# Optimization experiments

Hardware: AMD Instinct MI355X
Metric: run time of the kernel (lower is better)

The kernel has to match this reference:

```python
import jax, jax.numpy as jnp
import numpy as np

NEG_INF = -9e15
ALPHA = 2.0  # LeakyReLU negative slope from init (alpha=2)


def setup_inputs() -> dict:
    key = jax.random.key(0)
    k1, k2, k3, k4 = jax.random.split(key, 4)
    B, N, Fin, Fout = 8, 2048, 256, 128
    x = jax.random.normal(k1, (B, N, Fin), dtype=jnp.float32)
    adj = jax.random.randint(k2, (B, N, N), 0, 2, dtype=jnp.int32)
    # xavier_uniform with gain=1.414
    def xavier(k, shape, gain=1.414):
        fan_in, fan_out = shape[0], shape[1]
        bound = gain * np.sqrt(6.0 / (fan_in + fan_out))
        return jax.random.uniform(k, shape, jnp.float32, -bound, bound)
    W = xavier(k3, (Fin, Fout))
    a = xavier(k4, (2 * Fout, 1))
    return {"x": x, "adj": adj, "W": W, "a": a}


def reference(x, adj, W, a):
    # Wh: [B, N, Fout]
    Wh = jnp.matmul(x, W)
    Fout = W.shape[1]
    a1 = a[:Fout, 0]   # [Fout]
    a2 = a[Fout:, 0]   # [Fout]
    f1 = jnp.einsum('bnf,f->bn', Wh, a1)  # [B, N]
    f2 = jnp.einsum('bnf,f->bn', Wh, a2)  # [B, N]
    e = f1[:, :, None] + f2[:, None, :]   # [B, N, N]
    e = jnp.where(e >= 0, e, ALPHA * e)   # leaky relu, slope 2
    e = jnp.where(adj > 0, e, NEG_INF)
    attention = jax.nn.softmax(e, axis=2)
    # dropout: eval mode (no-op)
    h_prime = jnp.matmul(attention, Wh)   # [B, N, Fout]
    # concat=True -> elu
    return jnp.where(h_prime > 0, h_prime, jnp.expm1(h_prime))
```

## Files before the change

kernel.cpp:

```cpp
#include <hip/hip_runtime.h>
#include <hip/hip_bf16.h>
#include <math.h>

constexpr int B_   = 8;
constexpr int N_   = 2048;
constexpr int FIN  = 256;
constexpr int FOUT = 128;

constexpr int CH  = 512;
constexpr int NCH = N_ / CH;
constexpr int PR  = CH + 8;
constexpr int XR  = FIN + 8;
constexpr int TR  = 40;

typedef __attribute__((ext_vector_type(8))) short bf16x8;
typedef __attribute__((ext_vector_type(4))) float f32x4;
typedef __attribute__((ext_vector_type(4))) int   i32x4;

static __device__ __forceinline__ unsigned short f2bf(float f) {
    __hip_bfloat16 h = __float2bfloat16(f);
    return *reinterpret_cast<unsigned short*>(&h);
}
static __device__ __forceinline__ i32x4 ntload4(const int* p) {
    return __builtin_nontemporal_load((const i32x4*)p);
}

__global__ __launch_bounds__(256) void k0_wt(const float* __restrict__ W,
                                             unsigned short* __restrict__ Wt) {
    const int n = blockIdx.x;
    const int k = threadIdx.x;
    Wt[n * FIN + k] = f2bf(W[k * FOUT + n]);
}

__global__ __launch_bounds__(256) void ka_wh(const float* __restrict__ x,
                                             const unsigned short* __restrict__ Wt,
                                             const float* __restrict__ a,
                                             unsigned short* __restrict__ WhT,
                                             float* __restrict__ f1,
                                             float* __restrict__ f2) {
    __shared__ unsigned short xs[32 * XR];
    __shared__ float as[2 * FOUT];
    __shared__ float fred[2][4][32];

    const int tid = threadIdx.x;
    const int j0  = blockIdx.x * 32;
    const int b   = j0 >> 11;
    const int jb  = j0 & (N_ - 1);

    if (tid < 2 * FOUT) as[tid] = a[tid];
    {
        const float4* xsrc = (const float4*)(x + (size_t)j0 * FIN);
#pragma unroll
        for (int t = 0; t < 8; ++t) {
            const int idx = tid + t * 256;
            float4 v = xsrc[idx];
            const int row = idx >> 6, c4 = idx & 63;
            ushort4 u;
            u.x = f2bf(v.x); u.y = f2bf(v.y); u.z = f2bf(v.z); u.w = f2bf(v.w);
            *(ushort4*)&xs[row * XR + c4 * 4] = u;
        }
    }
    __syncthreads();

    const int wave = tid >> 6, lane = tid & 63;
    const int quad = lane >> 4, l16 = lane & 15;

    f32x4 acc[2][2];
#pragma unroll
    for (int aa = 0; aa < 2; ++aa)
#pragma unroll
        for (int nn = 0; nn < 2; ++nn) acc[aa][nn] = {0.f, 0.f, 0.f, 0.f};

    const unsigned short* wtA0 = Wt + (size_t)(32 * wave + l16) * FIN;
    const unsigned short* wtA1 = wtA0 + 16 * FIN;
#pragma unroll
    for (int ks = 0; ks < FIN / 32; ++ks) {
        const int kof = ks * 32 + quad * 8;
        bf16x8 af0 = *(const bf16x8*)&wtA0[kof];
        bf16x8 af1 = *(const bf16x8*)&wtA1[kof];
        bf16x8 bf0 = *(const bf16x8*)&xs[l16 * XR + kof];
        bf16x8 bf1 = *(const bf16x8*)&xs[(16 + l16) * XR + kof];
        acc[0][0] = __builtin_amdgcn_mfma_f32_16x16x32_bf16(af0, bf0, acc[0][0], 0, 0, 0);
        acc[0][1] = __builtin_amdgcn_mfma_f32_16x16x32_bf16(af0, bf1, acc[0][1], 0, 0, 0);
        acc[1][0] = __builtin_amdgcn_mfma_f32_16x16x32_bf16(af1, bf0, acc[1][0], 0, 0, 0);
        acc[1][1] = __builtin_amdgcn_mfma_f32_16x16x32_bf16(af1, bf1, acc[1][1], 0, 0, 0);
    }
    __syncthreads();

    unsigned short* T = xs;
    float pf[2][2] = {{0.f, 0.f}, {0.f, 0.f}};
#pragma unroll
    for (int aa = 0; aa < 2; ++aa)
#pragma unroll
        for (int nn = 0; nn < 2; ++nn)
#pragma unroll
            for (int r = 0; r < 4; ++r) {
                const int d = 32 * wave + 16 * aa + 4 * quad + r;
                const float v = acc[aa][nn][r];
                T[d * TR + nn * 16 + l16] = f2bf(v);
                pf[0][nn] += v * as[d];
                pf[1][nn] += v * as[FOUT + d];
            }
#pragma unroll
    for (int ff = 0; ff < 2; ++ff)
#pragma unroll
        for (int nn = 0; nn < 2; ++nn) {
            float v = pf[ff][nn];
            v += __shfl_xor(v, 16);
            v += __shfl_xor(v, 32);
            pf[ff][nn] = v;
        }
    if (quad == 0) {
#pragma unroll
        for (int ff = 0; ff < 2; ++ff)
#pragma unroll
            for (int nn = 0; nn < 2; ++nn)
                fred[ff][wave][nn * 16 + l16] = pf[ff][nn];
    }
    __syncthreads();

    unsigned short* dstW = WhT + (size_t)b * FOUT * N_;
#pragma unroll
    for (int it = 0; it < 2; ++it) {
        const int idx = it * 256 + tid;
        const int d = idx >> 2, q = idx & 3;
        bf16x8 v = *(const bf16x8*)&T[d * TR + q * 8];
        *(bf16x8*)&dstW[(size_t)d * N_ + jb + q * 8] = v;
    }
    if (tid < 64) {
        const int ff = tid >> 5, j32 = tid & 31;
        const float s = fred[ff][0][j32] + fred[ff][1][j32] +
                        fred[ff][2][j32] + fred[ff][3][j32];
        (ff ? f2 : f1)[(size_t)b * N_ + jb + j32] = s;
    }
}

static __device__ __forceinline__ void kb_phaseA(
    const int c, const int lane, const int wave, const int i0,
    const int* __restrict__ adjB, const float4* __restrict__ f2b4,
    const float* __restrict__ f1r, float* __restrict__ s_run,
    unsigned short* __restrict__ pb)
{
    const float4 fv0 = f2b4[c * (CH / 4) + lane];
    const float4 fv1 = f2b4[c * (CH / 4) + 64 + lane];
#pragma unroll
    for (int rr = 0; rr < 4; ++rr) {
        const int ti = wave * 4 + rr;
        const int i  = i0 + ti;
        const int* arow = adjB + (size_t)i * N_ + c * CH;
        const i32x4 av0 = ntload4(arow + 4 * lane);
        const i32x4 av1 = ntload4(arow + 256 + 4 * lane);
        const float f1i = f1r[rr];

        float e[8];
        e[0] = f1i + fv0.x; e[1] = f1i + fv0.y; e[2] = f1i + fv0.z; e[3] = f1i + fv0.w;
        e[4] = f1i + fv1.x; e[5] = f1i + fv1.y; e[6] = f1i + fv1.z; e[7] = f1i + fv1.w;
#pragma unroll
        for (int q = 0; q < 8; ++q) e[q] = (e[q] >= 0.f) ? e[q] : 2.f * e[q];

        float pv[8];
        pv[0] = (av0.x > 0) ? __expf(e[0]) : 0.f;
        pv[1] = (av0.y > 0) ? __expf(e[1]) : 0.f;
        pv[2] = (av0.z > 0) ? __expf(e[2]) : 0.f;
        pv[3] = (av0.w > 0) ? __expf(e[3]) : 0.f;
        pv[4] = (av1.x > 0) ? __expf(e[4]) : 0.f;
        pv[5] = (av1.y > 0) ? __expf(e[5]) : 0.f;
        pv[6] = (av1.z > 0) ? __expf(e[6]) : 0.f;
        pv[7] = (av1.w > 0) ? __expf(e[7]) : 0.f;

        s_run[rr] += ((pv[0] + pv[1]) + (pv[2] + pv[3])) +
                     ((pv[4] + pv[5]) + (pv[6] + pv[7]));

        ushort4 u0, u1;
        u0.x = f2bf(pv[0]); u0.y = f2bf(pv[1]); u0.z = f2bf(pv[2]); u0.w = f2bf(pv[3]);
        u1.x = f2bf(pv[4]); u1.y = f2bf(pv[5]); u1.z = f2bf(pv[6]); u1.w = f2bf(pv[7]);
        *(ushort4*)&pb[ti * PR + 4 * lane]       = u0;
        *(ushort4*)&pb[ti * PR + 256 + 4 * lane] = u1;
    }
}

__global__ __launch_bounds__(256) void kb_attn(const int* __restrict__ adj,
                                               const unsigned short* __restrict__ WhT,
                                               const float* __restrict__ f1,
                                               const float* __restrict__ f2,
                                               float* __restrict__ out) {
    __shared__ unsigned short p[2][16 * PR];
    __shared__ float rsum[16];

    const int tid  = threadIdx.x;
    const int b    = blockIdx.x & 7;
    const int i0   = (blockIdx.x >> 3) * 16;
    const int wave = tid >> 6, lane = tid & 63;
    const int quad = lane >> 4, l16 = lane & 15;

    const float4* f2b4 = (const float4*)(f2 + (size_t)b * N_);
    const int*    adjB = adj + (size_t)b * N_ * N_;

    float f1r[4], s_run[4];
#pragma unroll
    for (int rr = 0; rr < 4; ++rr) {
        f1r[rr]   = f1[(size_t)b * N_ + i0 + wave * 4 + rr];
        s_run[rr] = 0.f;
    }

    f32x4 acc0 = {0.f, 0.f, 0.f, 0.f}, acc1 = {0.f, 0.f, 0.f, 0.f};
    const int n0 = wave * 32;
    const unsigned short* wB0 = WhT + (size_t)b * FOUT * N_ + (size_t)(n0 + l16) * N_;
    const unsigned short* wB1 = wB0 + (size_t)16 * N_;

    kb_phaseA(0, lane, wave, i0, adjB, f2b4, f1r, s_run, &p[0][0]);
    __syncthreads();

    for (int c = 0; c < NCH; ++c) {
        if (c + 1 < NCH) {
            kb_phaseA(c + 1, lane, wave, i0, adjB, f2b4, f1r, s_run,
                      &p[(c + 1) & 1][0]);
        } else {
#pragma unroll
            for (int rr = 0; rr < 4; ++rr) {
                float s = s_run[rr];
#pragma unroll
                for (int o = 32; o; o >>= 1) s += __shfl_xor(s, o);
                if (lane == 0) rsum[wave * 4 + rr] = s;
            }
        }

        const unsigned short* pA = &p[c & 1][l16 * PR];
        const int kbase = c * CH;
#pragma unroll
        for (int ks = 0; ks < CH / 32; ++ks) {
            const int kof = ks * 32 + quad * 8;
            bf16x8 afr = *(const bf16x8*)&pA[kof];
            bf16x8 b0  = *(const bf16x8*)&wB0[kbase + kof];
            bf16x8 b1  = *(const bf16x8*)&wB1[kbase + kof];
            acc0 = __builtin_amdgcn_mfma_f32_16x16x32_bf16(afr, b0, acc0, 0, 0, 0);
            acc1 = __builtin_amdgcn_mfma_f32_16x16x32_bf16(afr, b1, acc1, 0, 0, 0);
        }
        __syncthreads();
    }

#pragma unroll
    for (int r = 0; r < 4; ++r) {
        const int m = quad * 4 + r;
        const float inv = 1.f / rsum[m];
        float v0 = acc0[r] * inv;
        float v1 = acc1[r] * inv;
        v0 = (v0 > 0.f) ? v0 : expm1f(v0);
        v1 = (v1 > 0.f) ? v1 : expm1f(v1);
        const size_t base = ((size_t)b * N_ + i0 + m) * FOUT + n0;
        out[base + l16]      = v0;
        out[base + 16 + l16] = v1;
    }
}

extern "C" void kernel_launch(void* const* d_in, const int* in_sizes, int n_in,
                              void* d_out, int out_size, void* d_ws, size_t ws_size,
                              hipStream_t stream) {
    const float* x   = (const float*)d_in[0];
    const int*   adj = (const int*)d_in[1];
    const float* W   = (const float*)d_in[2];
    const float* a   = (const float*)d_in[3];
    float* out = (float*)d_out;

    unsigned short* WhT = (unsigned short*)d_ws;
    unsigned short* Wt  = WhT + (size_t)B_ * FOUT * N_;
    float* f1 = (float*)(Wt + (size_t)FOUT * FIN);
    float* f2 = f1 + (size_t)B_ * N_;

    hipLaunchKernelGGL(k0_wt, dim3(FOUT), dim3(FIN), 0, stream, W, Wt);
    hipLaunchKernelGGL(ka_wh, dim3(B_ * N_ / 32), dim3(256), 0, stream,
                       x, Wt, a, WhT, f1, f2);
    hipLaunchKernelGGL(kb_attn, dim3(B_ * N_ / 16), dim3(256), 0, stream,
                       adj, WhT, f1, f2, out);
}
```

Measured before the change: 260.6 us.

## Split fused attention kernel into probability kernel and GEMM kernel via global P

Splits the fused softmax-numerator and attention-GEMM kernel into two launches. The first computes the masked exponentials and row sums and writes the bf16 probability matrix to a workspace. The second streams that matrix back into shared memory for the MFMA GEMM. This separates the memory-bound and compute phases, but it adds a full N×N bf16 write and read per batch through global memory.

```diff
diff --git a/kernel.cpp b/kernel.cpp
--- a/kernel.cpp
+++ b/kernel.cpp
@@ -135,57 +135,77 @@
     }
 }
 
-static __device__ __forceinline__ void kb_phaseA(
-    const int c, const int lane, const int wave, const int i0,
-    const int* __restrict__ adjB, const float4* __restrict__ f2b4,
-    const float* __restrict__ f1r, float* __restrict__ s_run,
-    unsigned short* __restrict__ pb)
-{
-    const float4 fv0 = f2b4[c * (CH / 4) + lane];
-    const float4 fv1 = f2b4[c * (CH / 4) + 64 + lane];
+__global__ __launch_bounds__(256) void kp_p(const int* __restrict__ adj,
+                                            const float* __restrict__ f1,
+                                            const float* __restrict__ f2,
+                                            unsigned short* __restrict__ P,
+                                            float* __restrict__ rsum) {
+    const int tid  = threadIdx.x;
+    const int b    = blockIdx.x & 7;
+    const int i0   = (blockIdx.x >> 3) * 16;
+    const int wave = tid >> 6, lane = tid & 63;
+
+    const float4* f2b4 = (const float4*)(f2 + (size_t)b * N_);
+    unsigned short* Pb = P + ((size_t)b * N_ + i0) * N_;
+
+    float f1r[4], s_run[4];
 #pragma unroll
     for (int rr = 0; rr < 4; ++rr) {
-        const int ti = wave * 4 + rr;
-        const int i  = i0 + ti;
-        const int* arow = adjB + (size_t)i * N_ + c * CH;
-        const i32x4 av0 = ntload4(arow + 4 * lane);
-        const i32x4 av1 = ntload4(arow + 256 + 4 * lane);
-        const float f1i = f1r[rr];
-
-        float e[8];
-        e[0] = f1i + fv0.x; e[1] = f1i + fv0.y; e[2] = f1i + fv0.z; e[3] = f1i + fv0.w;
-        e[4] = f1i + fv1.x; e[5] = f1i + fv1.y; e[6] = f1i + fv1.z; e[7] = f1i + fv1.w;
-#pragma unroll
-        for (int q = 0; q < 8; ++q) e[q] = (e[q] >= 0.f) ? e[q] : 2.f * e[q];
-
-        float pv[8];
-        pv[0] = (av0.x > 0) ? __expf(e[0]) : 0.f;
-        pv[1] = (av0.y > 0) ? __expf(e[1]) : 0.f;
-        pv[2] = (av0.z > 0) ? __expf(e[2]) : 0.f;
-        pv[3] = (av0.w > 0) ? __expf(e[3]) : 0.f;
-        pv[4] = (av1.x > 0) ? __expf(e[4]) : 0.f;
-        pv[5] = (av1.y > 0) ? __expf(e[5]) : 0.f;
-        pv[6] = (av1.z > 0) ? __expf(e[6]) : 0.f;
-        pv[7] = (av1.w > 0) ? __expf(e[7]) : 0.f;
-
-        s_run[rr] += ((pv[0] + pv[1]) + (pv[2] + pv[3])) +
-                     ((pv[4] + pv[5]) + (pv[6] + pv[7]));
-
-        ushort4 u0, u1;
-        u0.x = f2bf(pv[0]); u0.y = f2bf(pv[1]); u0.z = f2bf(pv[2]); u0.w = f2bf(pv[3]);
-        u1.x = f2bf(pv[4]); u1.y = f2bf(pv[5]); u1.z = f2bf(pv[6]); u1.w = f2bf(pv[7]);
-        *(ushort4*)&pb[ti * PR + 4 * lane]       = u0;
-        *(ushort4*)&pb[ti * PR + 256 + 4 * lane] = u1;
-    }
-}
-
-__global__ __launch_bounds__(256) void kb_attn(const int* __restrict__ adj,
+        f1r[rr]   = f1[(size_t)b * N_ + i0 + wave * 4 + rr];
+        s_run[rr] = 0.f;
+    }
+
+    for (int c = 0; c < NCH; ++c) {
+        const float4 fv0 = f2b4[c * (CH / 4) + lane];
+        const float4 fv1 = f2b4[c * (CH / 4) + 64 + lane];
+#pragma unroll
+        for (int rr = 0; rr < 4; ++rr) {
+            const int ti = wave * 4 + rr;
+            const int* arow = adj + ((size_t)b * N_ + i0 + ti) * N_ + c * CH;
+            const i32x4 av0 = ntload4(arow + 4 * lane);
+            const i32x4 av1 = ntload4(arow + 256 + 4 * lane);
+            const float f1i = f1r[rr];
+
+            float e[8];
+            e[0] = f1i + fv0.x; e[1] = f1i + fv0.y; e[2] = f1i + fv0.z; e[3] = f1i + fv0.w;
+            e[4] = f1i + fv1.x; e[5] = f1i + fv1.y; e[6] = f1i + fv1.z; e[7] = f1i + fv1.w;
+#pragma unroll
+            for (int q = 0; q < 8; ++q) e[q] = (e[q] >= 0.f) ? e[q] : 2.f * e[q];
+
+            float pv[8];
+            pv[0] = (av0.x > 0) ? __expf(e[0]) : 0.f;
+            pv[1] = (av0.y > 0) ? __expf(e[1]) : 0.f;
+            pv[2] = (av0.z > 0) ? __expf(e[2]) : 0.f;
+            pv[3] = (av0.w > 0) ? __expf(e[3]) : 0.f;
+            pv[4] = (av1.x > 0) ? __expf(e[4]) : 0.f;
+            pv[5] = (av1.y > 0) ? __expf(e[5]) : 0.f;
+            pv[6] = (av1.z > 0) ? __expf(e[6]) : 0.f;
+            pv[7] = (av1.w > 0) ? __expf(e[7]) : 0.f;
+            s_run[rr] += ((pv[0] + pv[1]) + (pv[2] + pv[3])) +
+                         ((pv[4] + pv[5]) + (pv[6] + pv[7]));
+
+            ushort4 u0, u1;
+            u0.x = f2bf(pv[0]); u0.y = f2bf(pv[1]); u0.z = f2bf(pv[2]); u0.w = f2bf(pv[3]);
+            u1.x = f2bf(pv[4]); u1.y = f2bf(pv[5]); u1.z = f2bf(pv[6]); u1.w = f2bf(pv[7]);
+            *(ushort4*)&Pb[(size_t)ti * N_ + c * CH + 4 * lane]       = u0;
+            *(ushort4*)&Pb[(size_t)ti * N_ + c * CH + 256 + 4 * lane] = u1;
+        }
+    }
+
+#pragma unroll
+    for (int rr = 0; rr < 4; ++rr) {
+        float s = s_run[rr];
+#pragma unroll
+        for (int o = 32; o; o >>= 1) s += __shfl_xor(s, o);
+        if (lane == 0) rsum[(size_t)b * N_ + i0 + wave * 4 + rr] = s;
+    }
+}
+
+__global__ __launch_bounds__(256) void kb_gemm(const unsigned short* __restrict__ P,
                                                const unsigned short* __restrict__ WhT,
-                                               const float* __restrict__ f1,
-                                               const float* __restrict__ f2,
+                                               const float* __restrict__ rsum,
                                                float* __restrict__ out) {
     __shared__ unsigned short p[2][16 * PR];
-    __shared__ float rsum[16];
 
     const int tid  = threadIdx.x;
     const int b    = blockIdx.x & 7;
@@ -193,35 +213,30 @@
     const int wave = tid >> 6, lane = tid & 63;
     const int quad = lane >> 4, l16 = lane & 15;
 
-    const float4* f2b4 = (const float4*)(f2 + (size_t)b * N_);
-    const int*    adjB = adj + (size_t)b * N_ * N_;
-
-    float f1r[4], s_run[4];
-#pragma unroll
-    for (int rr = 0; rr < 4; ++rr) {
-        f1r[rr]   = f1[(size_t)b * N_ + i0 + wave * 4 + rr];
-        s_run[rr] = 0.f;
-    }
-
-    f32x4 acc0 = {0.f, 0.f, 0.f, 0.f}, acc1 = {0.f, 0.f, 0.f, 0.f};
+    const unsigned short* Pb = P + ((size_t)b * N_ + i0) * N_;
+    const int srow = tid >> 4;
+    const int scol = (tid & 15) * 32;
+
     const int n0 = wave * 32;
     const unsigned short* wB0 = WhT + (size_t)b * FOUT * N_ + (size_t)(n0 + l16) * N_;
     const unsigned short* wB1 = wB0 + (size_t)16 * N_;
 
-    kb_phaseA(0, lane, wave, i0, adjB, f2b4, f1r, s_run, &p[0][0]);
+    f32x4 acc0 = {0.f, 0.f, 0.f, 0.f}, acc1 = {0.f, 0.f, 0.f, 0.f};
+
+#pragma unroll
+    for (int q = 0; q < 4; ++q) {
+        const bf16x8 v = *(const bf16x8*)&Pb[(size_t)srow * N_ + scol + q * 8];
+        *(bf16x8*)&p[0][srow * PR + scol + q * 8] = v;
+    }
     __syncthreads();
 
     for (int c = 0; c < NCH; ++c) {
         if (c + 1 < NCH) {
-            kb_phaseA(c + 1, lane, wave, i0, adjB, f2b4, f1r, s_run,
-                      &p[(c + 1) & 1][0]);
-        } else {
-#pragma unroll
-            for (int rr = 0; rr < 4; ++rr) {
-                float s = s_run[rr];
-#pragma unroll
-                for (int o = 32; o; o >>= 1) s += __shfl_xor(s, o);
-                if (lane == 0) rsum[wave * 4 + rr] = s;
+#pragma unroll
+            for (int q = 0; q < 4; ++q) {
+                const bf16x8 v =
+                    *(const bf16x8*)&Pb[(size_t)srow * N_ + (c + 1) * CH + scol + q * 8];
+                *(bf16x8*)&p[(c + 1) & 1][srow * PR + scol + q * 8] = v;
             }
         }
 
@@ -242,7 +257,7 @@
 #pragma unroll
     for (int r = 0; r < 4; ++r) {
         const int m = quad * 4 + r;
-        const float inv = 1.f / rsum[m];
+        const float inv = 1.f / rsum[(size_t)b * N_ + i0 + m];
         float v0 = acc0[r] * inv;
         float v1 = acc1[r] * inv;
         v0 = (v0 > 0.f) ? v0 : expm1f(v0);
@@ -264,12 +279,16 @@
 
     unsigned short* WhT = (unsigned short*)d_ws;
     unsigned short* Wt  = WhT + (size_t)B_ * FOUT * N_;
-    float* f1 = (float*)(Wt + (size_t)FOUT * FIN);
-    float* f2 = f1 + (size_t)B_ * N_;
+    float* f1   = (float*)(Wt + (size_t)FOUT * FIN);
+    float* f2   = f1 + (size_t)B_ * N_;
+    float* rsum = f2 + (size_t)B_ * N_;
+    unsigned short* P = (unsigned short*)(rsum + (size_t)B_ * N_);
 
     hipLaunchKernelGGL(k0_wt, dim3(FOUT), dim3(FIN), 0, stream, W, Wt);
     hipLaunchKernelGGL(ka_wh, dim3(B_ * N_ / 32), dim3(256), 0, stream,
                        x, Wt, a, WhT, f1, f2);
-    hipLaunchKernelGGL(kb_attn, dim3(B_ * N_ / 16), dim3(256), 0, stream,
-                       adj, WhT, f1, f2, out);
-}
+    hipLaunchKernelGGL(kp_p, dim3(B_ * N_ / 16), dim3(256), 0, stream,
+                       adj, f1, f2, P, rsum);
+    hipLaunchKernelGGL(kb_gemm, dim3(B_ * N_ / 16), dim3(256), 0, stream,
+                       P, WhT, rsum, out);
+}
```

Measured after the change: 296.1 us. +13.7%, slower.

## Split attention kernel into producer and consumer waves

Applied to the files above, without the earlier changes.

The attention kernel now launches 512 threads per block. Four producer waves compute masked exponentials from the adjacency rows into a double-buffered LDS tile, and four consumer waves run the MFMA product on the previous chunk. Before, the same waves did both phases in sequence. Specialising the waves is meant to overlap the memory-bound adjacency streaming with the matrix math. In exchange it doubles threads per block, keeps a block barrier every step, and can lower the number of resident blocks per CU because of register pressure.

```diff
diff --git a/kernel.cpp b/kernel.cpp
--- a/kernel.cpp
+++ b/kernel.cpp
@@ -136,7 +136,7 @@
 }
 
 static __device__ __forceinline__ void kb_phaseA(
-    const int c, const int lane, const int wave, const int i0,
+    const int c, const int lane, const int pw, const int i0,
     const int* __restrict__ adjB, const float4* __restrict__ f2b4,
     const float* __restrict__ f1r, float* __restrict__ s_run,
     unsigned short* __restrict__ pb)
@@ -145,7 +145,7 @@
     const float4 fv1 = f2b4[c * (CH / 4) + 64 + lane];
 #pragma unroll
     for (int rr = 0; rr < 4; ++rr) {
-        const int ti = wave * 4 + rr;
+        const int ti = pw * 4 + rr;
         const int i  = i0 + ti;
         const int* arow = adjB + (size_t)i * N_ + c * CH;
         const i32x4 av0 = ntload4(arow + 4 * lane);
@@ -167,7 +167,6 @@
         pv[5] = (av1.y > 0) ? __expf(e[5]) : 0.f;
         pv[6] = (av1.z > 0) ? __expf(e[6]) : 0.f;
         pv[7] = (av1.w > 0) ? __expf(e[7]) : 0.f;
-
         s_run[rr] += ((pv[0] + pv[1]) + (pv[2] + pv[3])) +
                      ((pv[4] + pv[5]) + (pv[6] + pv[7]));
 
@@ -179,19 +178,21 @@
     }
 }
 
-__global__ __launch_bounds__(256) void kb_attn(const int* __restrict__ adj,
-                                               const unsigned short* __restrict__ WhT,
-                                               const float* __restrict__ f1,
-                                               const float* __restrict__ f2,
-                                               float* __restrict__ out) {
+__global__ __launch_bounds__(512, 8) void kb_attn(const int* __restrict__ adj,
+                                                  const unsigned short* __restrict__ WhT,
+                                                  const float* __restrict__ f1,
+                                                  const float* __restrict__ f2,
+                                                  float* __restrict__ out) {
     __shared__ unsigned short p[2][16 * PR];
-    __shared__ float rsum[16];
+    __shared__ float rs[16];
 
     const int tid  = threadIdx.x;
     const int b    = blockIdx.x & 7;
     const int i0   = (blockIdx.x >> 3) * 16;
     const int wave = tid >> 6, lane = tid & 63;
     const int quad = lane >> 4, l16 = lane & 15;
+    const bool producer = (wave < 4);
+    const int  pw = wave & 3;
 
     const float4* f2b4 = (const float4*)(f2 + (size_t)b * N_);
     const int*    adjB = adj + (size_t)b * N_ * N_;
@@ -199,57 +200,59 @@
     float f1r[4], s_run[4];
 #pragma unroll
     for (int rr = 0; rr < 4; ++rr) {
-        f1r[rr]   = f1[(size_t)b * N_ + i0 + wave * 4 + rr];
+        f1r[rr]   = f1[(size_t)b * N_ + i0 + pw * 4 + rr];
         s_run[rr] = 0.f;
     }
 
     f32x4 acc0 = {0.f, 0.f, 0.f, 0.f}, acc1 = {0.f, 0.f, 0.f, 0.f};
-    const int n0 = wave * 32;
+    const int n0 = pw * 32;
     const unsigned short* wB0 = WhT + (size_t)b * FOUT * N_ + (size_t)(n0 + l16) * N_;
     const unsigned short* wB1 = wB0 + (size_t)16 * N_;
 
-    kb_phaseA(0, lane, wave, i0, adjB, f2b4, f1r, s_run, &p[0][0]);
-    __syncthreads();
-
-    for (int c = 0; c < NCH; ++c) {
-        if (c + 1 < NCH) {
-            kb_phaseA(c + 1, lane, wave, i0, adjB, f2b4, f1r, s_run,
-                      &p[(c + 1) & 1][0]);
-        } else {
-#pragma unroll
-            for (int rr = 0; rr < 4; ++rr) {
-                float s = s_run[rr];
-#pragma unroll
-                for (int o = 32; o; o >>= 1) s += __shfl_xor(s, o);
-                if (lane == 0) rsum[wave * 4 + rr] = s;
+    for (int step = 0; step <= NCH; ++step) {
+        if (producer) {
+            if (step < NCH) {
+                kb_phaseA(step, lane, pw, i0, adjB, f2b4, f1r, s_run,
+                          &p[step & 1][0]);
+            } else {
+#pragma unroll
+                for (int rr = 0; rr < 4; ++rr) {
+                    float s = s_run[rr];
+#pragma unroll
+                    for (int o = 32; o; o >>= 1) s += __shfl_xor(s, o);
+                    if (lane == 0) rs[pw * 4 + rr] = s;
+                }
             }
-        }
-
-        const unsigned short* pA = &p[c & 1][l16 * PR];
-        const int kbase = c * CH;
-#pragma unroll
-        for (int ks = 0; ks < CH / 32; ++ks) {
-            const int kof = ks * 32 + quad * 8;
-            bf16x8 afr = *(const bf16x8*)&pA[kof];
-            bf16x8 b0  = *(const bf16x8*)&wB0[kbase + kof];
-            bf16x8 b1  = *(const bf16x8*)&wB1[kbase + kof];
-            acc0 = __builtin_amdgcn_mfma_f32_16x16x32_bf16(afr, b0, acc0, 0, 0, 0);
-            acc1 = __builtin_amdgcn_mfma_f32_16x16x32_bf16(afr, b1, acc1, 0, 0, 0);
+        } else if (step >= 1) {
+            const int c = step - 1;
+            const unsigned short* pA = &p[c & 1][l16 * PR];
+            const int kbase = c * CH;
+#pragma unroll
+            for (int ks = 0; ks < CH / 32; ++ks) {
+                const int kof = ks * 32 + quad * 8;
+                bf16x8 afr = *(const bf16x8*)&pA[kof];
+                bf16x8 b0  = *(const bf16x8*)&wB0[kbase + kof];
+                bf16x8 b1  = *(const bf16x8*)&wB1[kbase + kof];
+                acc0 = __builtin_amdgcn_mfma_f32_16x16x32_bf16(afr, b0, acc0, 0, 0, 0);
+                acc1 = __builtin_amdgcn_mfma_f32_16x16x32_bf16(afr, b1, acc1, 0, 0, 0);
+            }
         }
         __syncthreads();
     }
 
-#pragma unroll
-    for (int r = 0; r < 4; ++r) {
-        const int m = quad * 4 + r;
-        const float inv = 1.f / rsum[m];
-        float v0 = acc0[r] * inv;
-        float v1 = acc1[r] * inv;
-        v0 = (v0 > 0.f) ? v0 : expm1f(v0);
-        v1 = (v1 > 0.f) ? v1 : expm1f(v1);
-        const size_t base = ((size_t)b * N_ + i0 + m) * FOUT + n0;
-        out[base + l16]      = v0;
-        out[base + 16 + l16] = v1;
+    if (!producer) {
+#pragma unroll
+        for (int r = 0; r < 4; ++r) {
+            const int m = quad * 4 + r;
+            const float inv = 1.f / rs[m];
+            float v0 = acc0[r] * inv;
+            float v1 = acc1[r] * inv;
+            v0 = (v0 > 0.f) ? v0 : expm1f(v0);
+            v1 = (v1 > 0.f) ? v1 : expm1f(v1);
+            const size_t base = ((size_t)b * N_ + i0 + m) * FOUT + n0;
+            out[base + l16]      = v0;
+            out[base + 16 + l16] = v1;
+        }
     }
 }
 
@@ -270,6 +273,6 @@
     hipLaunchKernelGGL(k0_wt, dim3(FOUT), dim3(FIN), 0, stream, W, Wt);
     hipLaunchKernelGGL(ka_wh, dim3(B_ * N_ / 32), dim3(256), 0, stream,
                        x, Wt, a, WhT, f1, f2);
-    hipLaunchKernelGGL(kb_attn, dim3(B_ * N_ / 16), dim3(256), 0, stream,
+    hipLaunchKernelGGL(kb_attn, dim3(B_ * N_ / 16), dim3(512), 0, stream,
                        adj, WhT, f1, f2, out);
 }
```

Result: slower. 268.2 us (+2.9%).
